# Optimization experiments

Hardware: AMD Instinct MI355X
Metric: run time of the kernel (lower is better)

The kernel has to match this reference:

```python
import jax, jax.numpy as jnp
import numpy as np

N_NODES = 50000
N_EDGES = 400000
NUM_FEATURES = 32
NUM_GRAPHS = 64
NUM_CLASSES = 2


def setup_inputs() -> dict:
    key = jax.random.key(0)
    ks = jax.random.split(key, 24)
    inp = {
        "x": jax.random.normal(ks[0], (N_NODES, NUM_FEATURES), dtype=jnp.float32),
        "edge_index": jax.random.randint(ks[1], (2, N_EDGES), 0, N_NODES),
        "edge_attr": jax.random.uniform(ks[2], (N_EDGES, 1), dtype=jnp.float32),
        "batch": jnp.sort(jax.random.randint(ks[3], (N_NODES,), 0, NUM_GRAPHS)),
        # nn1: Linear(1,10) -> ReLU -> Linear(10, 32*16)
        "nn1_w1": jax.random.normal(ks[4], (1, 10), dtype=jnp.float32) * 0.3,
        "nn1_b1": jnp.zeros((10,), jnp.float32),
        "nn1_w2": jax.random.normal(ks[5], (10, NUM_FEATURES * 16), dtype=jnp.float32) * 0.1,
        "nn1_b2": jnp.zeros((NUM_FEATURES * 16,), jnp.float32),
        "conv1_root": jax.random.normal(ks[6], (NUM_FEATURES, 16), dtype=jnp.float32) * 0.1,
        "conv1_bias": jnp.zeros((16,), jnp.float32),
        # nn2: Linear(1,10) -> ReLU -> Linear(10, 16*32)
        "nn2_w1": jax.random.normal(ks[7], (1, 10), dtype=jnp.float32) * 0.3,
        "nn2_b1": jnp.zeros((10,), jnp.float32),
        "nn2_w2": jax.random.normal(ks[8], (10, 16 * 32), dtype=jnp.float32) * 0.1,
        "nn2_b2": jnp.zeros((16 * 32,), jnp.float32),
        "conv2_root": jax.random.normal(ks[9], (16, 32), dtype=jnp.float32) * 0.15,
        "conv2_bias": jnp.zeros((32,), jnp.float32),
        "fc1_w": jax.random.normal(ks[10], (32, 64), dtype=jnp.float32) * 0.15,
        "fc1_b": jnp.zeros((64,), jnp.float32),
        "fc2_w": jax.random.normal(ks[11], (64, NUM_CLASSES), dtype=jnp.float32) * 0.1,
        "fc2_b": jnp.zeros((NUM_CLASSES,), jnp.float32),
    }
    return inp


def _nnconv(x, edge_src, edge_dst, edge_attr, w1, b1, w2, b2, root, bias, in_ch, out_ch):
    # Per-edge weight matrix from edge MLP: [E, in_ch, out_ch]
    h = jax.nn.relu(edge_attr @ w1 + b1) @ w2 + b2
    W = h.reshape(-1, in_ch, out_ch)
    msg = jnp.einsum('ei,eio->eo', x[edge_src], W)  # [E, out_ch]
    agg = jax.ops.segment_sum(msg, edge_dst, num_segments=N_NODES)
    cnt = jax.ops.segment_sum(jnp.ones((msg.shape[0],), x.dtype), edge_dst, num_segments=N_NODES)
    mean = agg / jnp.maximum(cnt, 1.0)[:, None]
    return mean + x @ root + bias


def reference(x, edge_index, edge_attr, batch,
              nn1_w1, nn1_b1, nn1_w2, nn1_b2, conv1_root, conv1_bias,
              nn2_w1, nn2_b1, nn2_w2, nn2_b2, conv2_root, conv2_bias,
              fc1_w, fc1_b, fc2_w, fc2_b):
    src, dst = edge_index[0], edge_index[1]
    h = jax.nn.elu(_nnconv(x, src, dst, edge_attr, nn1_w1, nn1_b1, nn1_w2, nn1_b2,
                           conv1_root, conv1_bias, NUM_FEATURES, 16))
    h = jax.nn.elu(_nnconv(h, src, dst, edge_attr, nn2_w1, nn2_b1, nn2_w2, nn2_b2,
                           conv2_root, conv2_bias, 16, 32))
    # global mean pool over graphs
    gsum = jax.ops.segment_sum(h, batch, num_segments=NUM_GRAPHS)
    gcnt = jax.ops.segment_sum(jnp.ones((h.shape[0],), h.dtype), batch, num_segments=NUM_GRAPHS)
    g = gsum / jnp.maximum(gcnt, 1.0)[:, None]
    g = jax.nn.elu(g @ fc1_w + fc1_b)
    return jax.nn.log_softmax(g @ fc2_w + fc2_b, axis=1)
```

## Files before the change

kernel.cpp:

```cpp
#include <hip/hip_runtime.h>
#include <hip/hip_fp16.h>
#include <math.h>

#define N_NODES 50000
#define N_EDGES 400000
#define NUM_GRAPHS 64


__global__ __launch_bounds__(256) void k1_p1(const float* __restrict__ x,
        const float* __restrict__ w2, const float* __restrict__ b2,
        const float* __restrict__ root, __half* __restrict__ P) {
    __shared__ float Wl[32][192];
    __shared__ float xl[16][32];
    int t = threadIdx.x;
    for (int idx = t; idx < 32 * 192; idx += 256) {
        int i = idx / 192, c = idx % 192;
        int m = c >> 4, o = c & 15;
        float w;
        if (m < 10)       w = w2[m * 512 + i * 16 + o];
        else if (m == 10) w = b2[i * 16 + o];
        else              w = root[i * 16 + o];
        Wl[i][c] = w;
    }
    int n0 = blockIdx.x * 16;
    for (int idx = t; idx < 16 * 32; idx += 256) {
        int nl = idx >> 5, i = idx & 31;
        int n = n0 + nl;
        xl[nl][i] = (n < N_NODES) ? x[n * 32 + i] : 0.f;
    }
    __syncthreads();
    int nl = t >> 4, o = t & 15;
    int n = n0 + nl;
    if (n >= N_NODES) return;
    float acc[12];
#pragma unroll
    for (int m = 0; m < 12; m++) acc[m] = 0.f;
#pragma unroll
    for (int i = 0; i < 32; i++) {
        float xv = xl[nl][i];
#pragma unroll
        for (int m = 0; m < 12; m++) acc[m] += xv * Wl[i][m * 16 + o];
    }
    __half2* Po = (__half2*)(P + (size_t)n * 192 + o * 12);
#pragma unroll
    for (int k = 0; k < 6; k++) Po[k] = __floats2half2_rn(acc[2 * k], acc[2 * k + 1]);
}

__global__ __launch_bounds__(256) void k4_p2(const float* __restrict__ agg1,
        const float* __restrict__ cnt, const __half* __restrict__ P1,
        const float* __restrict__ bias1,
        const float* __restrict__ w2, const float* __restrict__ b2,
        const float* __restrict__ root, __half* __restrict__ P2) {
    __shared__ float Wl[16][384];
    __shared__ float hl[8][16];
    int t = threadIdx.x;
    for (int idx = t; idx < 16 * 384; idx += 256) {
        int i = idx / 384, c = idx % 384;
        int m = c >> 5, o = c & 31;
        float w;
        if (m < 10)       w = w2[m * 512 + i * 32 + o];
        else if (m == 10) w = b2[i * 32 + o];
        else              w = root[i * 32 + o];
        Wl[i][c] = w;
    }
    int n0 = blockIdx.x * 8;
    if (t < 128) {
        int nl = t >> 4, i = t & 15;
        int n = n0 + nl;
        float v = 0.f;
        if (n < N_NODES) {
            float c = fmaxf(cnt[n], 1.0f);
            v = agg1[n * 16 + i] / c
              + __half2float(P1[(size_t)n * 192 + i * 12 + 11]) + bias1[i];
            v = v > 0.f ? v : expm1f(v);
        }
        hl[nl][i] = v;
    }
    __syncthreads();
    int nl = t >> 5, o = t & 31;
    int n = n0 + nl;
    if (n >= N_NODES) return;
    float acc[12];
#pragma unroll
    for (int m = 0; m < 12; m++) acc[m] = 0.f;
#pragma unroll
    for (int i = 0; i < 16; i++) {
        float hv = hl[nl][i];
#pragma unroll
        for (int m = 0; m < 12; m++) acc[m] += hv * Wl[i][m * 32 + o];
    }
    __half2* Po = (__half2*)(P2 + (size_t)n * 384 + o * 12);
#pragma unroll
    for (int k = 0; k < 6; k++) Po[k] = __floats2half2_rn(acc[2 * k], acc[2 * k + 1]);
}

__global__ __launch_bounds__(256) void k2_edge1(const __half* __restrict__ P,
        const int* __restrict__ src, const int* __restrict__ dst,
        const float* __restrict__ ea, const float* __restrict__ w1,
        const float* __restrict__ b1, float* __restrict__ agg,
        float* __restrict__ cnt) {
    int t = threadIdx.x;
    int e = blockIdx.x * 16 + (t >> 4);
    int o = t & 15;
    if (e >= N_EDGES) return;
    float a = ea[e];
    int s = src[e], d = dst[e];
    const float2* Pf = (const float2*)P;
    int base = s * 48 + o * 3;
    float2 f0 = Pf[base];
    float2 f1 = Pf[base + 1];
    float2 f2 = Pf[base + 2];
    float r[10];
#pragma unroll
    for (int j = 0; j < 10; j++) r[j] = fmaxf(a * w1[j] + b1[j], 0.f);
    union { float2 f; __half2 h[2]; } u;
    float m;
    {
        u.f = f2;
        float2 p89 = __half22float2(u.h[0]);
        float2 pQR = __half22float2(u.h[1]);
        m = pQR.x + r[8] * p89.x + r[9] * p89.y;
    }
    {
        u.f = f0;
        float2 p01 = __half22float2(u.h[0]);
        float2 p23 = __half22float2(u.h[1]);
        m += r[0] * p01.x + r[1] * p01.y + r[2] * p23.x + r[3] * p23.y;
    }
    {
        u.f = f1;
        float2 p45 = __half22float2(u.h[0]);
        float2 p67 = __half22float2(u.h[1]);
        m += r[4] * p45.x + r[5] * p45.y + r[6] * p67.x + r[7] * p67.y;
    }
    atomicAdd(agg + d * 16 + o, m);
    if (o == 0) atomicAdd(cnt + d, 1.0f);
}

__global__ __launch_bounds__(256) void k5_edge2(const __half* __restrict__ P,
        const int* __restrict__ src, const int* __restrict__ dst,
        const float* __restrict__ ea, const float* __restrict__ w1,
        const float* __restrict__ b1, float* __restrict__ agg) {
    int t = threadIdx.x;
    int e = blockIdx.x * 8 + (t >> 5);
    int o = t & 31;
    if (e >= N_EDGES) return;
    float a = ea[e];
    int s = src[e], d = dst[e];
    const float2* Pf = (const float2*)P;
    int base = s * 96 + o * 3;
    float2 f0 = Pf[base];
    float2 f1 = Pf[base + 1];
    float2 f2 = Pf[base + 2];
    float r[10];
#pragma unroll
    for (int j = 0; j < 10; j++) r[j] = fmaxf(a * w1[j] + b1[j], 0.f);
    union { float2 f; __half2 h[2]; } u;
    float m;
    {
        u.f = f2;
        float2 p89 = __half22float2(u.h[0]);
        float2 pQR = __half22float2(u.h[1]);
        m = pQR.x + r[8] * p89.x + r[9] * p89.y;
    }
    {
        u.f = f0;
        float2 p01 = __half22float2(u.h[0]);
        float2 p23 = __half22float2(u.h[1]);
        m += r[0] * p01.x + r[1] * p01.y + r[2] * p23.x + r[3] * p23.y;
    }
    {
        u.f = f1;
        float2 p45 = __half22float2(u.h[0]);
        float2 p67 = __half22float2(u.h[1]);
        m += r[4] * p45.x + r[5] * p45.y + r[6] * p67.x + r[7] * p67.y;
    }
    atomicAdd(agg + d * 32 + o, m);
}

__global__ __launch_bounds__(256) void k7_pool(const float* __restrict__ agg2,
        const float* __restrict__ cnt, const __half* __restrict__ P2,
        const float* __restrict__ bias2, const int* __restrict__ batch,
        float* __restrict__ gp) {
    int g = blockIdx.x;
    int t = threadIdx.x;
    int lo = 0, hi = N_NODES;
    while (lo < hi) { int mid = (lo + hi) >> 1; if (batch[mid] < g) lo = mid + 1; else hi = mid; }
    int start = lo;
    hi = N_NODES;
    while (lo < hi) { int mid = (lo + hi) >> 1; if (batch[mid] < g + 1) lo = mid + 1; else hi = mid; }
    int end = lo;
    int o = t & 31, ch = t >> 5;
    float s = 0.f;
    for (int n = start + ch; n < end; n += 8) {
        float c = fmaxf(cnt[n], 1.0f);
        float v = agg2[(size_t)n * 32 + o] / c
                + __half2float(P2[(size_t)n * 384 + o * 12 + 11]) + bias2[o];
        s += v > 0.f ? v : expm1f(v);
    }
    __shared__ float red[8][32];
    red[ch][o] = s;
    __syncthreads();
    if (t < 32) {
        float tot = 0.f;
#pragma unroll
        for (int c = 0; c < 8; c++) tot += red[c][t];
        gp[g * 32 + t] = tot / fmaxf((float)(end - start), 1.0f);
    }
}

__global__ __launch_bounds__(256) void k8_head(const float* __restrict__ gp,
        const float* __restrict__ fc1w, const float* __restrict__ fc1b,
        const float* __restrict__ fc2w, const float* __restrict__ fc2b,
        float* __restrict__ out) {
    __shared__ float gl[64][32];
    __shared__ float w1l[32][64];
    __shared__ float hl[64][64];
    __shared__ float zl[64][2];
    int t = threadIdx.x;
    for (int idx = t; idx < 64 * 32; idx += 256) gl[idx >> 5][idx & 31] = gp[idx];
    for (int idx = t; idx < 32 * 64; idx += 256) w1l[idx >> 6][idx & 63] = fc1w[idx];
    __syncthreads();
    for (int idx = t; idx < 64 * 64; idx += 256) {
        int gg = idx >> 6, c = idx & 63;
        float acc = fc1b[c];
#pragma unroll
        for (int i = 0; i < 32; i++) acc += gl[gg][i] * w1l[i][c];
        hl[gg][c] = acc > 0.f ? acc : expm1f(acc);
    }
    __syncthreads();
    if (t < 128) {
        int gg = t >> 1, k = t & 1;
        float acc = fc2b[k];
#pragma unroll
        for (int c = 0; c < 64; c++) acc += hl[gg][c] * fc2w[c * 2 + k];
        zl[gg][k] = acc;
    }
    __syncthreads();
    if (t < 128) {
        int gg = t >> 1, k = t & 1;
        float z0 = zl[gg][0], z1 = zl[gg][1];
        float m = fmaxf(z0, z1);
        float lse = m + logf(expf(z0 - m) + expf(z1 - m));
        out[t] = zl[gg][k] - lse;
    }
}

extern "C" void kernel_launch(void* const* d_in, const int* in_sizes, int n_in,
                              void* d_out, int out_size, void* d_ws, size_t ws_size,
                              hipStream_t stream) {
    const float* x       = (const float*)d_in[0];
    const int*   ei      = (const int*)d_in[1];
    const float* ea      = (const float*)d_in[2];
    const int*   batch   = (const int*)d_in[3];
    const float* nn1_w1  = (const float*)d_in[4];
    const float* nn1_b1  = (const float*)d_in[5];
    const float* nn1_w2  = (const float*)d_in[6];
    const float* nn1_b2  = (const float*)d_in[7];
    const float* c1_root = (const float*)d_in[8];
    const float* c1_bias = (const float*)d_in[9];
    const float* nn2_w1  = (const float*)d_in[10];
    const float* nn2_b1  = (const float*)d_in[11];
    const float* nn2_w2  = (const float*)d_in[12];
    const float* nn2_b2  = (const float*)d_in[13];
    const float* c2_root = (const float*)d_in[14];
    const float* c2_bias = (const float*)d_in[15];
    const float* fc1w    = (const float*)d_in[16];
    const float* fc1b    = (const float*)d_in[17];
    const float* fc2w    = (const float*)d_in[18];
    const float* fc2b    = (const float*)d_in[19];
    const int* src = ei;
    const int* dst = ei + N_EDGES;

    char* ws = (char*)d_ws;
    __half* P1 = (__half*)ws;
    __half* P2 = (__half*)(ws + (size_t)N_NODES * 192 * 2);
    float* fbase = (float*)(ws + (size_t)N_NODES * 192 * 2 + (size_t)N_NODES * 384 * 2);
    float* cnt  = fbase;
    float* agg1 = cnt + N_NODES;
    float* agg2 = agg1 + (size_t)N_NODES * 16;
    float* gp   = agg2 + (size_t)N_NODES * 32;

    hipMemsetAsync(cnt, 0, (size_t)(N_NODES + N_NODES * 16 + N_NODES * 32) * sizeof(float), stream);

    k1_p1<<<(N_NODES + 15) / 16, 256, 0, stream>>>(x, nn1_w2, nn1_b2, c1_root, P1);
    k2_edge1<<<(N_EDGES + 15) / 16, 256, 0, stream>>>(P1, src, dst, ea, nn1_w1, nn1_b1, agg1, cnt);
    k4_p2<<<(N_NODES + 7) / 8, 256, 0, stream>>>(agg1, cnt, P1, c1_bias, nn2_w2, nn2_b2, c2_root, P2);
    k5_edge2<<<(N_EDGES + 7) / 8, 256, 0, stream>>>(P2, src, dst, ea, nn2_w1, nn2_b1, agg2);
    k7_pool<<<NUM_GRAPHS, 256, 0, stream>>>(agg2, cnt, P2, c2_bias, batch, gp);
    k8_head<<<1, 256, 0, stream>>>(gp, fc1w, fc1b, fc2w, fc2b, (float*)d_out);
}
```

Before: 310.5 us.

## Split pooling across 512 blocks with atomics and store root terms in fp32

```diff
diff --git a/kernel.cpp b/kernel.cpp
--- a/kernel.cpp
+++ b/kernel.cpp
@@ -9,7 +9,8 @@
 
 __global__ __launch_bounds__(256) void k1_p1(const float* __restrict__ x,
         const float* __restrict__ w2, const float* __restrict__ b2,
-        const float* __restrict__ root, __half* __restrict__ P) {
+        const float* __restrict__ root, __half* __restrict__ P,
+        float* __restrict__ R1) {
     __shared__ float Wl[32][192];
     __shared__ float xl[16][32];
     int t = threadIdx.x;
@@ -44,13 +45,15 @@
     __half2* Po = (__half2*)(P + (size_t)n * 192 + o * 12);
 #pragma unroll
     for (int k = 0; k < 6; k++) Po[k] = __floats2half2_rn(acc[2 * k], acc[2 * k + 1]);
+    R1[n * 16 + o] = acc[11];
 }
 
 __global__ __launch_bounds__(256) void k4_p2(const float* __restrict__ agg1,
-        const float* __restrict__ cnt, const __half* __restrict__ P1,
+        const float* __restrict__ cnt, const float* __restrict__ R1,
         const float* __restrict__ bias1,
         const float* __restrict__ w2, const float* __restrict__ b2,
-        const float* __restrict__ root, __half* __restrict__ P2) {
+        const float* __restrict__ root, __half* __restrict__ P2,
+        float* __restrict__ R2) {
     __shared__ float Wl[16][384];
     __shared__ float hl[8][16];
     int t = threadIdx.x;
@@ -70,8 +73,7 @@
         float v = 0.f;
         if (n < N_NODES) {
             float c = fmaxf(cnt[n], 1.0f);
-            v = agg1[n * 16 + i] / c
-              + __half2float(P1[(size_t)n * 192 + i * 12 + 11]) + bias1[i];
+            v = agg1[n * 16 + i] / c + R1[n * 16 + i] + bias1[i];
             v = v > 0.f ? v : expm1f(v);
         }
         hl[nl][i] = v;
@@ -92,6 +94,7 @@
     __half2* Po = (__half2*)(P2 + (size_t)n * 384 + o * 12);
 #pragma unroll
     for (int k = 0; k < 6; k++) Po[k] = __floats2half2_rn(acc[2 * k], acc[2 * k + 1]);
+    R2[(size_t)n * 32 + o] = acc[11];
 }
 
 __global__ __launch_bounds__(256) void k2_edge1(const __half* __restrict__ P,
@@ -178,38 +181,36 @@
     atomicAdd(agg + d * 32 + o, m);
 }
 
-__global__ __launch_bounds__(256) void k7_pool(const float* __restrict__ agg2,
-        const float* __restrict__ cnt, const __half* __restrict__ P2,
+__global__ __launch_bounds__(256) void k6_partial(const float* __restrict__ agg2,
+        const float* __restrict__ cnt, const float* __restrict__ R2,
         const float* __restrict__ bias2, const int* __restrict__ batch,
-        float* __restrict__ gp) {
-    int g = blockIdx.x;
-    int t = threadIdx.x;
-    int lo = 0, hi = N_NODES;
-    while (lo < hi) { int mid = (lo + hi) >> 1; if (batch[mid] < g) lo = mid + 1; else hi = mid; }
-    int start = lo;
-    hi = N_NODES;
-    while (lo < hi) { int mid = (lo + hi) >> 1; if (batch[mid] < g + 1) lo = mid + 1; else hi = mid; }
-    int end = lo;
+        float* __restrict__ gsum) {
+    const int NB = 512;
+    const int chunk = (N_NODES + NB - 1) / NB;
+    int begin = blockIdx.x * chunk;
+    int end = begin + chunk;
+    if (end > N_NODES) end = N_NODES;
+    int t = threadIdx.x;
     int o = t & 31, ch = t >> 5;
-    float s = 0.f;
-    for (int n = start + ch; n < end; n += 8) {
+    float bz = bias2[o];
+    float acc = 0.f;
+    int cur_g = -1;
+    for (int n = begin + ch; n < end; n += 8) {
+        int g = batch[n];
         float c = fmaxf(cnt[n], 1.0f);
-        float v = agg2[(size_t)n * 32 + o] / c
-                + __half2float(P2[(size_t)n * 384 + o * 12 + 11]) + bias2[o];
-        s += v > 0.f ? v : expm1f(v);
-    }
-    __shared__ float red[8][32];
-    red[ch][o] = s;
-    __syncthreads();
-    if (t < 32) {
-        float tot = 0.f;
-#pragma unroll
-        for (int c = 0; c < 8; c++) tot += red[c][t];
-        gp[g * 32 + t] = tot / fmaxf((float)(end - start), 1.0f);
-    }
-}
-
-__global__ __launch_bounds__(256) void k8_head(const float* __restrict__ gp,
+        float v = agg2[(size_t)n * 32 + o] / c + R2[(size_t)n * 32 + o] + bz;
+        v = v > 0.f ? v : expm1f(v);
+        if (g != cur_g) {
+            if (cur_g >= 0) atomicAdd(gsum + cur_g * 32 + o, acc);
+            cur_g = g; acc = 0.f;
+        }
+        acc += v;
+    }
+    if (cur_g >= 0) atomicAdd(gsum + cur_g * 32 + o, acc);
+}
+
+__global__ __launch_bounds__(256) void k8_head(const float* __restrict__ gsum,
+        const int* __restrict__ batch,
         const float* __restrict__ fc1w, const float* __restrict__ fc1b,
         const float* __restrict__ fc2w, const float* __restrict__ fc2b,
         float* __restrict__ out) {
@@ -217,9 +218,20 @@
     __shared__ float w1l[32][64];
     __shared__ float hl[64][64];
     __shared__ float zl[64][2];
-    int t = threadIdx.x;
-    for (int idx = t; idx < 64 * 32; idx += 256) gl[idx >> 5][idx & 31] = gp[idx];
+    __shared__ float gc[64];
+    int t = threadIdx.x;
+    if (t < 64) {
+        int g = t;
+        int lo = 0, hi = N_NODES;
+        while (lo < hi) { int mid = (lo + hi) >> 1; if (batch[mid] < g) lo = mid + 1; else hi = mid; }
+        int s0 = lo;
+        lo = 0; hi = N_NODES;
+        while (lo < hi) { int mid = (lo + hi) >> 1; if (batch[mid] < g + 1) lo = mid + 1; else hi = mid; }
+        gc[g] = fmaxf((float)(lo - s0), 1.0f);
+    }
     for (int idx = t; idx < 32 * 64; idx += 256) w1l[idx >> 6][idx & 63] = fc1w[idx];
+    __syncthreads();
+    for (int idx = t; idx < 64 * 32; idx += 256) gl[idx >> 5][idx & 31] = gsum[idx] / gc[idx >> 5];
     __syncthreads();
     for (int idx = t; idx < 64 * 64; idx += 256) {
         int gg = idx >> 6, c = idx & 63;
@@ -279,14 +291,17 @@
     float* cnt  = fbase;
     float* agg1 = cnt + N_NODES;
     float* agg2 = agg1 + (size_t)N_NODES * 16;
-    float* gp   = agg2 + (size_t)N_NODES * 32;
-
-    hipMemsetAsync(cnt, 0, (size_t)(N_NODES + N_NODES * 16 + N_NODES * 32) * sizeof(float), stream);
-
-    k1_p1<<<(N_NODES + 15) / 16, 256, 0, stream>>>(x, nn1_w2, nn1_b2, c1_root, P1);
+    float* gsum = agg2 + (size_t)N_NODES * 32;
+    float* R1   = gsum + NUM_GRAPHS * 32;
+    float* R2   = R1 + (size_t)N_NODES * 16;
+
+    hipMemsetAsync(cnt, 0,
+        (size_t)(N_NODES + N_NODES * 16 + N_NODES * 32 + NUM_GRAPHS * 32) * sizeof(float), stream);
+
+    k1_p1<<<(N_NODES + 15) / 16, 256, 0, stream>>>(x, nn1_w2, nn1_b2, c1_root, P1, R1);
     k2_edge1<<<(N_EDGES + 15) / 16, 256, 0, stream>>>(P1, src, dst, ea, nn1_w1, nn1_b1, agg1, cnt);
-    k4_p2<<<(N_NODES + 7) / 8, 256, 0, stream>>>(agg1, cnt, P1, c1_bias, nn2_w2, nn2_b2, c2_root, P2);
+    k4_p2<<<(N_NODES + 7) / 8, 256, 0, stream>>>(agg1, cnt, R1, c1_bias, nn2_w2, nn2_b2, c2_root, P2, R2);
     k5_edge2<<<(N_EDGES + 7) / 8, 256, 0, stream>>>(P2, src, dst, ea, nn2_w1, nn2_b1, agg2);
-    k7_pool<<<NUM_GRAPHS, 256, 0, stream>>>(agg2, cnt, P2, c2_bias, batch, gp);
-    k8_head<<<1, 256, 0, stream>>>(gp, fc1w, fc1b, fc2w, fc2b, (float*)d_out);
-}
+    k6_partial<<<512, 256, 0, stream>>>(agg2, cnt, R2, c2_bias, batch, gsum);
+    k8_head<<<1, 256, 0, stream>>>(gsum, batch, fc1w, fc1b, fc2w, fc2b, (float*)d_out);
+}
```

New measurement: 281.8 us. 9.2% less time.
